# Kernel optimization log

Hardware: AMD Instinct MI355X
Metric: run time of the kernel (lower is better)

## Reference

```python
import jax, jax.numpy as jnp
import numpy as np
from jax import lax

EPS = 1e-5
DN = ('NCHW', 'OIHW', 'NCHW')

def _sign(v):
    # (v >= 0) * 2 - 1
    return jnp.where(v >= 0, 1.0, -1.0).astype(v.dtype)

def _conv(x, w, b):
    y = lax.conv_general_dilated(x, w, (1, 1), 'VALID', dimension_numbers=DN)
    return y + b[None, :, None, None]

def _bn(x):
    # BatchNorm2d(affine=False), training mode: biased batch stats over (N,H,W)
    m = jnp.mean(x, axis=(0, 2, 3), keepdims=True)
    v = jnp.var(x, axis=(0, 2, 3), keepdims=True)
    return (x - m) * lax.rsqrt(v + EPS)

def setup_inputs() -> dict:
    key = jax.random.key(0)
    ks = jax.random.split(key, 9)
    f = jnp.float32
    B = 8192
    x = jax.random.normal(ks[0], (B, 1, 28, 28), dtype=f)
    # conv params, clipped to [-1, 1] as in clip_weights()
    w1 = jnp.clip(jax.random.normal(ks[1], (32, 1, 9, 9), dtype=f) * 0.1, -1, 1)
    b1 = jnp.clip(jax.random.normal(ks[2], (32,), dtype=f) * 0.1, -1, 1)
    w2 = jnp.clip(jax.random.normal(ks[3], (16, 32, 9, 9), dtype=f) * 0.1, -1, 1)
    b2 = jnp.clip(jax.random.normal(ks[4], (16,), dtype=f) * 0.1, -1, 1)
    w3 = jnp.clip(jax.random.normal(ks[5], (8, 16, 9, 9), dtype=f) * 0.1, -1, 1)
    b3 = jnp.clip(jax.random.normal(ks[6], (8,), dtype=f) * 0.1, -1, 1)
    wl = jnp.clip(jax.random.normal(ks[7], (10, 8, 4, 4), dtype=f) * 0.1, -1, 1)
    bl = jnp.clip(jax.random.normal(ks[8], (10,), dtype=f) * 0.1, -1, 1)
    return {"x": x, "w1": w1, "b1": b1, "w2": w2, "b2": b2,
            "w3": w3, "b3": b3, "wl": wl, "bl": bl}

def _block(x, w, b, act=True, norm=True, binarized=True):
    if binarized:
        w, b = _sign(w), _sign(b)
    x = _conv(x, w, b)
    if norm:
        x = _bn(x)
    if act:
        x = _sign(x) if binarized else jax.nn.relu(x)
    return x

def reference(x, w1, b1, w2, b2, w3, b3, wl, bl):
    x = _sign(x)                        # binarize input activations
    x = _block(x, w1, b1)               # (B, 32, 20, 20)
    x = _block(x, w2, b2)               # (B, 16, 12, 12)
    x = _block(x, w3, b3)               # (B,  8,  4,  4)
    x = _block(x, wl, bl, act=False, norm=False)  # (B, 10, 1, 1), binarized weights
    return x.reshape(-1, 10)
```

## Files before the change

### kernel.cpp

```cpp
#include <hip/hip_runtime.h>
#include <stdint.h>

#define BATCH 8192

#define OFF_W1R3   0
#define OFF_W2P    384
#define OFF_W3P    6144
#define OFF_WLB    9600
#define OFF_SBL    9760
#define OFF_TTOT   9856
#define OFF_S3     10184
#define OFF_S2PART 10496
#define OFF_Z2     76800
#define OFF_Z3     37825792

__global__ __launch_bounds__(256) void k1_pack_tsum(const float* __restrict__ x,
                                                    const float* __restrict__ w1,
                                                    const float* __restrict__ w2,
                                                    const float* __restrict__ w3,
                                                    const float* __restrict__ wl,
                                                    const float* __restrict__ bl,
                                                    uint8_t* __restrict__ ws) {
  int* Ttot = (int*)(ws + OFF_TTOT);
  const int tid = threadIdx.x;

  if (blockIdx.x == 0) {
    uint32_t* W1R3 = (uint32_t*)(ws + OFF_W1R3);
    uint32_t* W2P  = (uint32_t*)(ws + OFF_W2P);
    uint32_t* W3P  = (uint32_t*)(ws + OFF_W3P);
    uint64_t* WLB  = (uint64_t*)(ws + OFF_WLB);
    float*    SBL  = (float*)(ws + OFF_SBL);
    for (int e = tid; e < 96; e += 256) {
      int oc = e / 3, i = e % 3;
      uint32_t m = 0;
      for (int rr = 0; rr < 3; ++rr)
        for (int kw = 0; kw < 9; ++kw)
          if (w1[oc*81 + (3*i+rr)*9 + kw] < 0.f) m |= 1u << (rr*9 + kw);
      W1R3[e] = m;
    }
    for (int e = tid; e < 648; e += 256) {
      int och = e / 81, k = e % 81;
      int kh = k / 9, kw = k % 9;
      uint32_t m0 = 0, m1 = 0;
      int oc0 = och*2;
      for (int ic = 0; ic < 32; ++ic) {
        if (w2[(oc0*32 + ic)*81 + k] < 0.f)     m0 |= 1u << ic;
        if (w2[((oc0+1)*32 + ic)*81 + k] < 0.f) m1 |= 1u << ic;
      }
      int idx = ((och*9 + kh)*10 + kw)*2;
      W2P[idx] = m0; W2P[idx+1] = m1;
    }
    for (int e = tid; e < 72; e += 256) {
      int idx = (e*10 + 9)*2;
      W2P[idx] = 0; W2P[idx+1] = 0;
    }
    for (int e = tid; e < 648; e += 256) {
      int oc = e / 81, k = e % 81;
      int kh = k / 9, kw = k % 9;
      uint32_t m = 0;
      for (int ic = 0; ic < 16; ++ic)
        if (w3[(oc*16 + ic)*81 + k] < 0.f) m |= 1u << ic;
      W3P[(oc*9 + kh)*12 + kw] = m;
    }
    for (int e = tid; e < 216; e += 256) {
      int row = e / 3, p = e % 3;
      W3P[row*12 + 9 + p] = 0;
    }
    for (int e = tid; e < 20; e += 256) {
      int oc = e >> 1, word = e & 1;
      uint64_t m = 0;
      for (int b = 0; b < 64; ++b)
        if (wl[oc*128 + word*64 + b] < 0.f) m |= 1ull << b;
      WLB[e] = m;
    }
    if (tid < 10) SBL[tid] = (bl[tid] >= 0.f) ? 1.f : -1.f;
  }

  __shared__ uint32_t rowm[224];
  __shared__ int Tacc[81];
  if (tid < 81) Tacc[tid] = 0;
  __syncthreads();

  const int img0 = blockIdx.x * 8;
  if (tid < 224) {
    int il = tid / 28, r = tid % 28;
    const float4* xr = (const float4*)(x + (size_t)(img0 + il) * 784 + r * 28);
    uint32_t m = 0;
    #pragma unroll
    for (int j = 0; j < 7; ++j) {
      float4 v = xr[j];
      if (v.x < 0.f) m |= 1u << (j*4+0);
      if (v.y < 0.f) m |= 1u << (j*4+1);
      if (v.z < 0.f) m |= 1u << (j*4+2);
      if (v.w < 0.f) m |= 1u << (j*4+3);
    }
    rowm[tid] = m;
  }
  __syncthreads();

  if (tid < 72) {
    int il = tid / 9, kw = tid % 9;
    int base = il * 28;
    int n9[9];
    int sum20 = 0;
    #pragma unroll
    for (int r = 0; r < 20; ++r) {
      int n = __popc((rowm[base + r] >> kw) & 0xFFFFFu);
      if (r < 9) n9[r] = n;
      sum20 += n;
    }
    atomicAdd(&Tacc[kw], 400 - 2*sum20);
    #pragma unroll
    for (int kh = 1; kh <= 8; ++kh) {
      int nadd = __popc((rowm[base + kh + 19] >> kw) & 0xFFFFFu);
      sum20 += nadd - n9[kh-1];
      atomicAdd(&Tacc[kh*9 + kw], 400 - 2*sum20);
    }
  }
  __syncthreads();
  if (tid < 81) atomicAdd(&Ttot[tid], Tacc[tid]);
}

#define K2_IMGS 8
__global__ __launch_bounds__(256) void k2_conv12(const float* __restrict__ x,
                                                 uint8_t* __restrict__ ws) {
  const uint32_t* W1R3g = (const uint32_t*)(ws + OFF_W1R3);
  const uint32_t* W2Pg  = (const uint32_t*)(ws + OFF_W2P);
  const int* Ttot = (const int*)(ws + OFF_TTOT);
  int* S2P = (int*)(ws + OFF_S2PART);

  __shared__ uint32_t __attribute__((aligned(16))) rowm[K2_IMGS*28];
  __shared__ uint32_t __attribute__((aligned(16))) w1r3[96];
  __shared__ uint32_t __attribute__((aligned(16))) w2p[1440];
  __shared__ int tlds[81];
  __shared__ int t1s[32];
  __shared__ uint32_t __attribute__((aligned(16))) A1s[K2_IMGS*400];
  __shared__ int s2acc[16];

  const int tid = threadIdx.x;
  const int img0 = blockIdx.x * K2_IMGS;

  for (int e = tid; e < 96; e += 256)   w1r3[e] = W1R3g[e];
  for (int e = tid; e < 1440; e += 256) w2p[e]  = W2Pg[e];
  if (tid < 81) tlds[tid] = Ttot[tid];
  if (tid < 16) s2acc[tid] = 0;
  if (tid < K2_IMGS*28) {
    int il = tid / 28, rr = tid % 28;
    const float4* xr = (const float4*)(x + (size_t)(img0 + il) * 784 + rr * 28);
    uint32_t m = 0;
    #pragma unroll
    for (int j = 0; j < 7; ++j) {
      float4 v = xr[j];
      if (v.x < 0.f) m |= 1u << (j*4+0);
      if (v.y < 0.f) m |= 1u << (j*4+1);
      if (v.z < 0.f) m |= 1u << (j*4+2);
      if (v.w < 0.f) m |= 1u << (j*4+3);
    }
    rowm[tid] = m;
  }
  __syncthreads();

  if (tid < 32) {
    long long S = 0;
    for (int kh = 0; kh < 9; ++kh)
      for (int kw = 0; kw < 9; ++kw) {
        int bit = (w1r3[tid*3 + kh/3] >> ((kh%3)*9 + kw)) & 1;
        S += (long long)(1 - 2*bit) * tlds[kh*9 + kw];
      }
    const long long N1 = (long long)BATCH * 400;
    long long q = S / N1, rr = S % N1;
    long long t = q + (rr > 0 ? 1 : 0);
    if ((t & 1) == 0) t += 1;
    t1s[tid] = (int)t;
  }
  __syncthreads();

  for (int G = tid; G < K2_IMGS*80; G += 256) {
    int il = G / 80, rem = G - il*80;
    int oh = rem >> 2, ow0 = (rem & 3) * 5;
    uint32_t R[9];
    #pragma unroll
    for (int i = 0; i < 9; ++i) R[i] = rowm[il*28 + oh + i];
    uint32_t win[5][3];
    #pragma unroll
    for (int j = 0; j < 5; ++j) {
      int ow = ow0 + j;
      #pragma unroll
      for (int i = 0; i < 3; ++i) {
        uint32_t b0 = (R[3*i]   >> ow) & 0x1FFu;
        uint32_t b1 = (R[3*i+1] >> ow) & 0x1FFu;
        uint32_t b2 = (R[3*i+2] >> ow) & 0x1FFu;
        win[j][i] = b0 | (b1 << 9) | (b2 << 18);
      }
    }
    uint32_t mask[5] = {0,0,0,0,0};
    #pragma unroll
    for (int ocg = 0; ocg < 4; ++ocg) {
      const uint4* wp = (const uint4*)&w1r3[ocg*24];
      uint32_t wr[24];
      #pragma unroll
      for (int q = 0; q < 6; ++q) {
        uint4 v = wp[q];
        wr[q*4+0]=v.x; wr[q*4+1]=v.y; wr[q*4+2]=v.z; wr[q*4+3]=v.w;
      }
      #pragma unroll
      for (int o8 = 0; o8 < 8; ++o8) {
        int oc = ocg*8 + o8;
        int t = t1s[oc];
        #pragma unroll
        for (int j = 0; j < 5; ++j) {
          int mm = __popc(win[j][0] ^ wr[o8*3])
                 + __popc(win[j][1] ^ wr[o8*3+1])
                 + __popc(win[j][2] ^ wr[o8*3+2]);
          mask[j] |= (uint32_t)((81 - 2*mm) < t) << oc;
        }
      }
    }
    #pragma unroll
    for (int j = 0; j < 5; ++j) A1s[il*400 + oh*20 + ow0 + j] = mask[j];
  }
  __syncthreads();

  uint32_t* Z2w = (uint32_t*)(ws + OFF_Z2);
  const int och = tid & 7, oc0 = och << 1;
  int sl0 = 0, sl1 = 0;
  for (int r = 0; r < 3; ++r) {
    int G = tid + r*256;
    int il = G / 96, rem = G - il*96;
    int oy = rem >> 3;
    const uint32_t* A = &A1s[il*400 + oy*20];
    int acc0[12], acc1[12];
    #pragma unroll
    for (int p = 0; p < 12; ++p) { acc0[p] = 0; acc1[p] = 0; }
    for (int kh = 0; kh < 9; ++kh) {
      const uint4* ar = (const uint4*)(A + kh*20);
      uint32_t a[20];
      #pragma unroll
      for (int q = 0; q < 5; ++q) {
        uint4 v = ar[q];
        a[q*4+0]=v.x; a[q*4+1]=v.y; a[q*4+2]=v.z; a[q*4+3]=v.w;
      }
      const uint4* wp4 = (const uint4*)&w2p[(och*9 + kh)*20];
      uint32_t wbuf[20];
      #pragma unroll
      for (int q = 0; q < 5; ++q) {
        uint4 v = wp4[q];
        wbuf[q*4+0]=v.x; wbuf[q*4+1]=v.y; wbuf[q*4+2]=v.z; wbuf[q*4+3]=v.w;
      }
      #pragma unroll
      for (int kw = 0; kw < 9; ++kw) {
        uint32_t w0 = wbuf[2*kw], w1v = wbuf[2*kw+1];
        #pragma unroll
        for (int px = 0; px < 12; ++px) {
          acc0[px] += __popc(a[kw+px] ^ w0);
          acc1[px] += __popc(a[kw+px] ^ w1v);
        }
      }
    }
    size_t wbase = (size_t)(img0+il)*1152 + (size_t)oy*96 + och;
    #pragma unroll
    for (int px = 0; px < 12; ++px) {
      int z0 = 2592 - 2*acc0[px], z1v = 2592 - 2*acc1[px];
      sl0 += z0; sl1 += z1v;
      Z2w[wbase + px*8] = (uint32_t)(uint16_t)(int16_t)z0
                        | ((uint32_t)(uint16_t)(int16_t)z1v << 16);
    }
  }
  atomicAdd(&s2acc[oc0],   sl0);
  atomicAdd(&s2acc[oc0+1], sl1);
  __syncthreads();
  if (tid < 16) S2P[blockIdx.x*16 + tid] = s2acc[tid];
}

#define K3_IMGS 8
__global__ __launch_bounds__(256) void k3_conv3(uint8_t* __restrict__ ws) {
  const int* S2P = (const int*)(ws + OFF_S2PART);
  const uint32_t* W3Pg = (const uint32_t*)(ws + OFF_W3P);
  const uint32_t* Z2w = (const uint32_t*)(ws + OFF_Z2);
  uint32_t* Z3w = (uint32_t*)(ws + OFF_Z3);
  unsigned long long* S3 = (unsigned long long*)(ws + OFF_S3);

  __shared__ uint32_t __attribute__((aligned(16))) w3p[864];
  __shared__ int part[256];
  __shared__ int t2s[16];
  __shared__ uint32_t __attribute__((aligned(16))) A2[K3_IMGS*144];
  __shared__ int s3acc[8];

  const int tid = threadIdx.x;
  const int img0 = blockIdx.x * K3_IMGS;

  {
    int c = tid & 15, g = tid >> 4;
    int s = 0;
    for (int j = 0; j < 64; ++j) s += S2P[(g + 16*j)*16 + c];
    part[tid] = s;
  }
  for (int e = tid; e < 864; e += 256) w3p[e] = W3Pg[e];
  if (tid < 8) s3acc[tid] = 0;
  __syncthreads();
  if (tid < 16) {
    long long S = 0;
    #pragma unroll
    for (int g = 0; g < 16; ++g) S += (long long)part[g*16 + tid];
    const long long N2 = (long long)BATCH * 144;
    long long q = S / N2, r = S % N2;
    long long t = q + (r > 0 ? 1 : 0);
    if (t & 1) t += 1;
    t2s[tid] = (int)t;
  }
  __syncthreads();

  for (int idx = tid; idx < K3_IMGS*144; idx += 256) {
    const uint4* zp = (const uint4*)&Z2w[(size_t)(img0 + idx/144)*1152 + (size_t)(idx%144)*8];
    uint4 v0 = zp[0], v1 = zp[1];
    uint32_t zz[8] = {v0.x,v0.y,v0.z,v0.w, v1.x,v1.y,v1.z,v1.w};
    uint32_t m = 0;
    #pragma unroll
    for (int i = 0; i < 8; ++i) {
      int zlo = (int)(short)(zz[i] & 0xFFFFu);
      int zhi = (int)zz[i] >> 16;
      m |= (uint32_t)(zlo < t2s[2*i])   << (2*i);
      m |= (uint32_t)(zhi < t2s[2*i+1]) << (2*i+1);
    }
    A2[idx] = m;
  }
  __syncthreads();

  const int il = tid >> 5, oc = (tid >> 2) & 7, oy = tid & 3;
  int acc[4] = {0, 0, 0, 0};
  #pragma unroll
  for (int kh = 0; kh < 9; ++kh) {
    const uint4* ar = (const uint4*)&A2[il*144 + (oy + kh)*12];
    uint4 v0 = ar[0], v1 = ar[1], v2 = ar[2];
    uint32_t a[12] = {v0.x,v0.y,v0.z,v0.w, v1.x,v1.y,v1.z,v1.w, v2.x,v2.y,v2.z,v2.w};
    const uint4* wr = (const uint4*)&w3p[(oc*9 + kh)*12];
    uint4 w0 = wr[0], w1v = wr[1], w2v = wr[2];
    uint32_t w[9] = {w0.x,w0.y,w0.z,w0.w, w1v.x,w1v.y,w1v.z,w1v.w, w2v.x};
    #pragma unroll
    for (int ox = 0; ox < 4; ++ox) {
      #pragma unroll
      for (int kw = 0; kw < 9; ++kw) acc[ox] += __popc(a[ox+kw] ^ w[kw]);
    }
  }
  int ssum = 0;
  uint32_t packed[2];
  #pragma unroll
  for (int h = 0; h < 2; ++h) {
    int za = 1296 - 2*acc[2*h], zb = 1296 - 2*acc[2*h+1];
    ssum += za + zb;
    packed[h] = (uint32_t)(uint16_t)(int16_t)za | ((uint32_t)(uint16_t)(int16_t)zb << 16);
  }
  *(uint2*)&Z3w[(size_t)(img0 + il)*64 + oc*8 + oy*2] = make_uint2(packed[0], packed[1]);
  atomicAdd(&s3acc[oc], ssum);
  __syncthreads();
  if (tid < 8)
    atomicAdd(&S3[tid], (unsigned long long)(long long)s3acc[tid]);
}

__global__ __launch_bounds__(64) void k4_final(uint8_t* __restrict__ ws,
                                               float* __restrict__ out) {
  const uint32_t* Z3w = (const uint32_t*)(ws + OFF_Z3);
  const long long* S3 = (const long long*)(ws + OFF_S3);
  const uint64_t* WLBg = (const uint64_t*)(ws + OFF_WLB);
  const float* SBLg = (const float*)(ws + OFF_SBL);
  __shared__ int t3[8];
  __shared__ uint64_t wlb[20];
  __shared__ float sbl[10];
  const int tid = threadIdx.x;
  if (tid < 8) {
    long long S = S3[tid];
    const long long N3 = (long long)BATCH * 16;
    long long q = S / N3, r = S % N3;
    long long t = q + (r > 0 ? 1 : 0);
    if (t & 1) t += 1;
    t3[tid] = (int)t;
  }
  if (tid < 20) wlb[tid] = WLBg[tid];
  if (tid < 10) sbl[tid] = SBLg[tid];
  __syncthreads();
  int img = blockIdx.x * 64 + tid;
  const uint4* zp = (const uint4*)&Z3w[(size_t)img * 64];
  uint32_t zz[64];
  #pragma unroll
  for (int q = 0; q < 16; ++q) {
    uint4 v = zp[q];
    zz[q*4+0]=v.x; zz[q*4+1]=v.y; zz[q*4+2]=v.z; zz[q*4+3]=v.w;
  }
  uint64_t a0 = 0, a1 = 0;
  #pragma unroll
  for (int j = 0; j < 64; ++j) {
    int z = (j & 1) ? ((int)zz[j>>1] >> 16) : (int)(short)(zz[j>>1] & 0xFFFFu);
    a0 |= (uint64_t)(z < t3[j >> 4]) << j;
  }
  #pragma unroll
  for (int j = 0; j < 64; ++j) {
    int z = (j & 1) ? ((int)zz[32 + (j>>1)] >> 16) : (int)(short)(zz[32 + (j>>1)] & 0xFFFFu);
    a1 |= (uint64_t)(z < t3[(64 + j) >> 4]) << j;
  }
  #pragma unroll
  for (int oc = 0; oc < 10; ++oc) {
    int mism = __popcll(a0 ^ wlb[oc*2]) + __popcll(a1 ^ wlb[oc*2 + 1]);
    out[(size_t)img*10 + oc] = (float)(128 - 2*mism) + sbl[oc];
  }
}

extern "C" void kernel_launch(void* const* d_in, const int* in_sizes, int n_in,
                              void* d_out, int out_size, void* d_ws, size_t ws_size,
                              hipStream_t stream) {
  (void)in_sizes; (void)n_in; (void)out_size; (void)ws_size;
  const float* x  = (const float*)d_in[0];
  const float* w1 = (const float*)d_in[1];
  const float* w2 = (const float*)d_in[3];
  const float* w3 = (const float*)d_in[5];
  const float* wl = (const float*)d_in[7];
  const float* bl = (const float*)d_in[8];
  uint8_t* ws = (uint8_t*)d_ws;
  float* out = (float*)d_out;

  hipMemsetAsync(ws + OFF_TTOT, 0, 400, stream);
  k1_pack_tsum<<<1024, 256, 0, stream>>>(x, w1, w2, w3, wl, bl, ws);
  k2_conv12<<<1024, 256, 0, stream>>>(x, ws);
  k3_conv3<<<1024, 256, 0, stream>>>(ws);
  k4_final<<<128, 64, 0, stream>>>(ws, out);
}
```

Measured before the change: 272.4 us.

## Fuse four BNN kernels into one cooperative persistent kernel with grid syncs

Replaces the four separate kernel launches and the memset with a single cooperative kernel. Blocks loop over virtual blocks and use grid.sync between the phases that need global batch-norm statistics. Global atomics for the stats are replaced by per-block partial arrays that each block reduces after the sync, and weight packing is split across four blocks. This removes launch gaps and the memset, at the cost of grid-wide barriers, redundant partial reductions in every block, and a shared-memory union sized for the largest phase, which may lower occupancy.

```diff
diff --git a/kernel.cpp b/kernel.cpp
--- a/kernel.cpp
+++ b/kernel.cpp
@@ -1,35 +1,74 @@
 #include <hip/hip_runtime.h>
+#include <hip/hip_cooperative_groups.h>
 #include <stdint.h>
 
+namespace cg = cooperative_groups;
+
 #define BATCH 8192
-
-#define OFF_W1R3   0
-#define OFF_W2P    384
-#define OFF_W3P    6144
-#define OFF_WLB    9600
-#define OFF_SBL    9760
-#define OFF_TTOT   9856
-#define OFF_S3     10184
-#define OFF_S2PART 10496
-#define OFF_Z2     76800
-#define OFF_Z3     37825792
-
-__global__ __launch_bounds__(256) void k1_pack_tsum(const float* __restrict__ x,
-                                                    const float* __restrict__ w1,
-                                                    const float* __restrict__ w2,
-                                                    const float* __restrict__ w3,
-                                                    const float* __restrict__ wl,
-                                                    const float* __restrict__ bl,
-                                                    uint8_t* __restrict__ ws) {
-  int* Ttot = (int*)(ws + OFF_TTOT);
+#define NVB   1024
+
+#define OFF_W1R3  0
+#define OFF_W2P   384
+#define OFF_W3P   6144
+#define OFF_WLB   9600
+#define OFF_SBL   9760
+#define OFF_TPART 9856
+#define OFF_S2P   341632
+#define OFF_S3P   407168
+#define OFF_Z2    440320
+#define OFF_Z3    38189056
+
+struct PhaseA { uint32_t rowm[224]; int Tacc[81]; };
+struct PhaseB { uint32_t rowm[224]; uint32_t w1r3[96]; uint32_t w2p[1440];
+                int red[256]; int tlds[81]; int t1s[32];
+                uint32_t A1s[3200]; int s2acc[16]; };
+struct PhaseC { uint32_t w3p[864]; int part[256]; int t2s[16]; int s3acc[8];
+                uint32_t A2[1152]; };
+struct PhaseD { int red[128]; int t3[8]; uint64_t wlb[20]; float sbl[10]; };
+union SMemU { PhaseA a; PhaseB b; PhaseC c; PhaseD d; };
+
+__global__ __launch_bounds__(256)
+void fused_bnn(const float* __restrict__ x,  const float* __restrict__ w1,
+               const float* __restrict__ w2, const float* __restrict__ w3,
+               const float* __restrict__ wl, const float* __restrict__ bl,
+               uint8_t* __restrict__ ws, float* __restrict__ out) {
+  cg::grid_group grid = cg::this_grid();
+  __shared__ __align__(16) SMemU sm;
   const int tid = threadIdx.x;
+  const int G = gridDim.x;
+
+  int* TPART = (int*)(ws + OFF_TPART);
+  int* S2P   = (int*)(ws + OFF_S2P);
+  int* S3P   = (int*)(ws + OFF_S3P);
+  uint32_t* Z2w = (uint32_t*)(ws + OFF_Z2);
+  uint32_t* Z3w = (uint32_t*)(ws + OFF_Z3);
 
   if (blockIdx.x == 0) {
+    uint32_t* W2P = (uint32_t*)(ws + OFF_W2P);
+    for (int e = tid; e < 648; e += 256) {
+      int och = e / 81, k = e % 81, kh = k / 9, kw = k % 9;
+      uint32_t m0 = 0, m1 = 0;
+      int oc0 = och * 2;
+      for (int ic = 0; ic < 32; ++ic) {
+        if (w2[(oc0*32 + ic)*81 + k] < 0.f)     m0 |= 1u << ic;
+        if (w2[((oc0+1)*32 + ic)*81 + k] < 0.f) m1 |= 1u << ic;
+      }
+      int idx = ((och*9 + kh)*10 + kw)*2;
+      W2P[idx] = m0; W2P[idx+1] = m1;
+    }
+    for (int e = tid; e < 72; e += 256) { int idx = (e*10 + 9)*2; W2P[idx] = 0; W2P[idx+1] = 0; }
+  } else if (blockIdx.x == 1) {
+    uint32_t* W3P = (uint32_t*)(ws + OFF_W3P);
+    for (int e = tid; e < 648; e += 256) {
+      int oc = e / 81, k = e % 81, kh = k / 9, kw = k % 9;
+      uint32_t m = 0;
+      for (int ic = 0; ic < 16; ++ic)
+        if (w3[(oc*16 + ic)*81 + k] < 0.f) m |= 1u << ic;
+      W3P[(oc*9 + kh)*12 + kw] = m;
+    }
+    for (int e = tid; e < 216; e += 256) { int row = e / 3, p = e % 3; W3P[row*12 + 9 + p] = 0; }
+  } else if (blockIdx.x == 2) {
     uint32_t* W1R3 = (uint32_t*)(ws + OFF_W1R3);
-    uint32_t* W2P  = (uint32_t*)(ws + OFF_W2P);
-    uint32_t* W3P  = (uint32_t*)(ws + OFF_W3P);
-    uint64_t* WLB  = (uint64_t*)(ws + OFF_WLB);
-    float*    SBL  = (float*)(ws + OFF_SBL);
     for (int e = tid; e < 96; e += 256) {
       int oc = e / 3, i = e % 3;
       uint32_t m = 0;
@@ -38,34 +77,9 @@
           if (w1[oc*81 + (3*i+rr)*9 + kw] < 0.f) m |= 1u << (rr*9 + kw);
       W1R3[e] = m;
     }
-    for (int e = tid; e < 648; e += 256) {
-      int och = e / 81, k = e % 81;
-      int kh = k / 9, kw = k % 9;
-      uint32_t m0 = 0, m1 = 0;
-      int oc0 = och*2;
-      for (int ic = 0; ic < 32; ++ic) {
-        if (w2[(oc0*32 + ic)*81 + k] < 0.f)     m0 |= 1u << ic;
-        if (w2[((oc0+1)*32 + ic)*81 + k] < 0.f) m1 |= 1u << ic;
-      }
-      int idx = ((och*9 + kh)*10 + kw)*2;
-      W2P[idx] = m0; W2P[idx+1] = m1;
-    }
-    for (int e = tid; e < 72; e += 256) {
-      int idx = (e*10 + 9)*2;
-      W2P[idx] = 0; W2P[idx+1] = 0;
-    }
-    for (int e = tid; e < 648; e += 256) {
-      int oc = e / 81, k = e % 81;
-      int kh = k / 9, kw = k % 9;
-      uint32_t m = 0;
-      for (int ic = 0; ic < 16; ++ic)
-        if (w3[(oc*16 + ic)*81 + k] < 0.f) m |= 1u << ic;
-      W3P[(oc*9 + kh)*12 + kw] = m;
-    }
-    for (int e = tid; e < 216; e += 256) {
-      int row = e / 3, p = e % 3;
-      W3P[row*12 + 9 + p] = 0;
-    }
+  } else if (blockIdx.x == 3) {
+    uint64_t* WLB = (uint64_t*)(ws + OFF_WLB);
+    float* SBL = (float*)(ws + OFF_SBL);
     for (int e = tid; e < 20; e += 256) {
       int oc = e >> 1, word = e & 1;
       uint64_t m = 0;
@@ -76,331 +90,328 @@
     if (tid < 10) SBL[tid] = (bl[tid] >= 0.f) ? 1.f : -1.f;
   }
 
-  __shared__ uint32_t rowm[224];
-  __shared__ int Tacc[81];
-  if (tid < 81) Tacc[tid] = 0;
-  __syncthreads();
-
-  const int img0 = blockIdx.x * 8;
-  if (tid < 224) {
-    int il = tid / 28, r = tid % 28;
-    const float4* xr = (const float4*)(x + (size_t)(img0 + il) * 784 + r * 28);
-    uint32_t m = 0;
-    #pragma unroll
-    for (int j = 0; j < 7; ++j) {
-      float4 v = xr[j];
-      if (v.x < 0.f) m |= 1u << (j*4+0);
-      if (v.y < 0.f) m |= 1u << (j*4+1);
-      if (v.z < 0.f) m |= 1u << (j*4+2);
-      if (v.w < 0.f) m |= 1u << (j*4+3);
-    }
-    rowm[tid] = m;
+  for (int vb = blockIdx.x; vb < NVB; vb += G) {
+    if (tid < 81) sm.a.Tacc[tid] = 0;
+    __syncthreads();
+    const int img0 = vb * 8;
+    if (tid < 224) {
+      int il = tid / 28, r = tid % 28;
+      const float4* xr = (const float4*)(x + (size_t)(img0 + il) * 784 + r * 28);
+      uint32_t m = 0;
+      #pragma unroll
+      for (int j = 0; j < 7; ++j) {
+        float4 v = xr[j];
+        if (v.x < 0.f) m |= 1u << (j*4+0);
+        if (v.y < 0.f) m |= 1u << (j*4+1);
+        if (v.z < 0.f) m |= 1u << (j*4+2);
+        if (v.w < 0.f) m |= 1u << (j*4+3);
+      }
+      sm.a.rowm[tid] = m;
+    }
+    __syncthreads();
+    if (tid < 72) {
+      int il = tid / 9, kw = tid % 9;
+      int base = il * 28;
+      int n9[9];
+      int sum20 = 0;
+      #pragma unroll
+      for (int r = 0; r < 20; ++r) {
+        int n = __popc((sm.a.rowm[base + r] >> kw) & 0xFFFFFu);
+        if (r < 9) n9[r] = n;
+        sum20 += n;
+      }
+      atomicAdd(&sm.a.Tacc[kw], 400 - 2*sum20);
+      #pragma unroll
+      for (int kh = 1; kh <= 8; ++kh) {
+        int nadd = __popc((sm.a.rowm[base + kh + 19] >> kw) & 0xFFFFFu);
+        sum20 += nadd - n9[kh-1];
+        atomicAdd(&sm.a.Tacc[kh*9 + kw], 400 - 2*sum20);
+      }
+    }
+    __syncthreads();
+    if (tid < 81) TPART[vb*81 + tid] = sm.a.Tacc[tid];
+    __syncthreads();
   }
-  __syncthreads();
-
-  if (tid < 72) {
-    int il = tid / 9, kw = tid % 9;
-    int base = il * 28;
-    int n9[9];
-    int sum20 = 0;
-    #pragma unroll
-    for (int r = 0; r < 20; ++r) {
-      int n = __popc((rowm[base + r] >> kw) & 0xFFFFFu);
-      if (r < 9) n9[r] = n;
-      sum20 += n;
-    }
-    atomicAdd(&Tacc[kw], 400 - 2*sum20);
-    #pragma unroll
-    for (int kh = 1; kh <= 8; ++kh) {
-      int nadd = __popc((rowm[base + kh + 19] >> kw) & 0xFFFFFu);
-      sum20 += nadd - n9[kh-1];
-      atomicAdd(&Tacc[kh*9 + kw], 400 - 2*sum20);
-    }
+  __threadfence();
+  grid.sync();
+
+  {
+    const uint32_t* W1R3g = (const uint32_t*)(ws + OFF_W1R3);
+    const uint32_t* W2Pg  = (const uint32_t*)(ws + OFF_W2P);
+    for (int e = tid; e < 96; e += 256)   sm.b.w1r3[e] = W1R3g[e];
+    for (int e = tid; e < 1440; e += 256) sm.b.w2p[e]  = W2Pg[e];
+    {
+      int s = 0;
+      if (tid < 243) {
+        int k = tid % 81, sub = tid / 81;
+        for (int r = sub; r < NVB; r += 3) s += TPART[r*81 + k];
+      }
+      sm.b.red[tid] = s;
+    }
+    __syncthreads();
+    if (tid < 81) sm.b.tlds[tid] = sm.b.red[tid] + sm.b.red[tid+81] + sm.b.red[tid+162];
+    __syncthreads();
+    if (tid < 32) {
+      long long S = 0;
+      for (int kh = 0; kh < 9; ++kh)
+        for (int kw = 0; kw < 9; ++kw) {
+          int bit = (sm.b.w1r3[tid*3 + kh/3] >> ((kh%3)*9 + kw)) & 1;
+          S += (long long)(1 - 2*bit) * sm.b.tlds[kh*9 + kw];
+        }
+      const long long N1 = (long long)BATCH * 400;
+      long long q = S / N1, rr = S % N1;
+      long long t = q + (rr > 0 ? 1 : 0);
+      if ((t & 1) == 0) t += 1;
+      sm.b.t1s[tid] = (int)t;
+    }
+    if (tid < 16) sm.b.s2acc[tid] = 0;
+    __syncthreads();
+
+    const int och = tid & 7, oc0 = och << 1;
+    for (int vb = blockIdx.x; vb < NVB; vb += G) {
+      const int img0 = vb * 8;
+      if (tid < 224) {
+        int il = tid / 28, rr = tid % 28;
+        const float4* xr = (const float4*)(x + (size_t)(img0 + il) * 784 + rr * 28);
+        uint32_t m = 0;
+        #pragma unroll
+        for (int j = 0; j < 7; ++j) {
+          float4 v = xr[j];
+          if (v.x < 0.f) m |= 1u << (j*4+0);
+          if (v.y < 0.f) m |= 1u << (j*4+1);
+          if (v.z < 0.f) m |= 1u << (j*4+2);
+          if (v.w < 0.f) m |= 1u << (j*4+3);
+        }
+        sm.b.rowm[tid] = m;
+      }
+      __syncthreads();
+
+      for (int Gt = tid; Gt < 640; Gt += 256) {
+        int il = Gt / 80, rem = Gt - il*80;
+        int oh = rem >> 2, ow0 = (rem & 3) * 5;
+        uint32_t R[9];
+        #pragma unroll
+        for (int i = 0; i < 9; ++i) R[i] = sm.b.rowm[il*28 + oh + i];
+        uint32_t win[5][3];
+        #pragma unroll
+        for (int j = 0; j < 5; ++j) {
+          int ow = ow0 + j;
+          #pragma unroll
+          for (int i = 0; i < 3; ++i) {
+            uint32_t b0 = (R[3*i]   >> ow) & 0x1FFu;
+            uint32_t b1 = (R[3*i+1] >> ow) & 0x1FFu;
+            uint32_t b2 = (R[3*i+2] >> ow) & 0x1FFu;
+            win[j][i] = b0 | (b1 << 9) | (b2 << 18);
+          }
+        }
+        uint32_t mask[5] = {0,0,0,0,0};
+        #pragma unroll
+        for (int ocg = 0; ocg < 4; ++ocg) {
+          const uint4* wp = (const uint4*)&sm.b.w1r3[ocg*24];
+          uint32_t wr[24];
+          #pragma unroll
+          for (int q = 0; q < 6; ++q) {
+            uint4 v = wp[q];
+            wr[q*4+0]=v.x; wr[q*4+1]=v.y; wr[q*4+2]=v.z; wr[q*4+3]=v.w;
+          }
+          #pragma unroll
+          for (int o8 = 0; o8 < 8; ++o8) {
+            int oc = ocg*8 + o8;
+            int t = sm.b.t1s[oc];
+            #pragma unroll
+            for (int j = 0; j < 5; ++j) {
+              int mm = __popc(win[j][0] ^ wr[o8*3])
+                     + __popc(win[j][1] ^ wr[o8*3+1])
+                     + __popc(win[j][2] ^ wr[o8*3+2]);
+              mask[j] |= (uint32_t)((81 - 2*mm) < t) << oc;
+            }
+          }
+        }
+        #pragma unroll
+        for (int j = 0; j < 5; ++j) sm.b.A1s[il*400 + oh*20 + ow0 + j] = mask[j];
+      }
+      __syncthreads();
+
+      int sl0 = 0, sl1 = 0;
+      for (int r = 0; r < 3; ++r) {
+        int Gt = tid + r*256;
+        int il = Gt / 96, rem = Gt - il*96;
+        int oy = rem >> 3;
+        const uint32_t* A = &sm.b.A1s[il*400 + oy*20];
+        int acc0[12], acc1[12];
+        #pragma unroll
+        for (int p = 0; p < 12; ++p) { acc0[p] = 0; acc1[p] = 0; }
+        for (int kh = 0; kh < 9; ++kh) {
+          const uint4* ar = (const uint4*)(A + kh*20);
+          uint32_t a[20];
+          #pragma unroll
+          for (int q = 0; q < 5; ++q) {
+            uint4 v = ar[q];
+            a[q*4+0]=v.x; a[q*4+1]=v.y; a[q*4+2]=v.z; a[q*4+3]=v.w;
+          }
+          const uint4* wp4 = (const uint4*)&sm.b.w2p[(och*9 + kh)*20];
+          uint32_t wbuf[20];
+          #pragma unroll
+          for (int q = 0; q < 5; ++q) {
+            uint4 v = wp4[q];
+            wbuf[q*4+0]=v.x; wbuf[q*4+1]=v.y; wbuf[q*4+2]=v.z; wbuf[q*4+3]=v.w;
+          }
+          #pragma unroll
+          for (int kw = 0; kw < 9; ++kw) {
+            uint32_t w0 = wbuf[2*kw], w1v = wbuf[2*kw+1];
+            #pragma unroll
+            for (int px = 0; px < 12; ++px) {
+              acc0[px] += __popc(a[kw+px] ^ w0);
+              acc1[px] += __popc(a[kw+px] ^ w1v);
+            }
+          }
+        }
+        size_t wbase = (size_t)(img0+il)*1152 + (size_t)oy*96 + och;
+        #pragma unroll
+        for (int px = 0; px < 12; ++px) {
+          int z0 = 2592 - 2*acc0[px], z1v = 2592 - 2*acc1[px];
+          sl0 += z0; sl1 += z1v;
+          Z2w[wbase + px*8] = (uint32_t)(uint16_t)(int16_t)z0
+                            | ((uint32_t)(uint16_t)(int16_t)z1v << 16);
+        }
+      }
+      atomicAdd(&sm.b.s2acc[oc0],   sl0);
+      atomicAdd(&sm.b.s2acc[oc0+1], sl1);
+      __syncthreads();
+    }
+    if (tid < 16) S2P[blockIdx.x*16 + tid] = sm.b.s2acc[tid];
   }
-  __syncthreads();
-  if (tid < 81) atomicAdd(&Ttot[tid], Tacc[tid]);
-}
-
-#define K2_IMGS 8
-__global__ __launch_bounds__(256) void k2_conv12(const float* __restrict__ x,
-                                                 uint8_t* __restrict__ ws) {
-  const uint32_t* W1R3g = (const uint32_t*)(ws + OFF_W1R3);
-  const uint32_t* W2Pg  = (const uint32_t*)(ws + OFF_W2P);
-  const int* Ttot = (const int*)(ws + OFF_TTOT);
-  int* S2P = (int*)(ws + OFF_S2PART);
-
-  __shared__ uint32_t __attribute__((aligned(16))) rowm[K2_IMGS*28];
-  __shared__ uint32_t __attribute__((aligned(16))) w1r3[96];
-  __shared__ uint32_t __attribute__((aligned(16))) w2p[1440];
-  __shared__ int tlds[81];
-  __shared__ int t1s[32];
-  __shared__ uint32_t __attribute__((aligned(16))) A1s[K2_IMGS*400];
-  __shared__ int s2acc[16];
-
-  const int tid = threadIdx.x;
-  const int img0 = blockIdx.x * K2_IMGS;
-
-  for (int e = tid; e < 96; e += 256)   w1r3[e] = W1R3g[e];
-  for (int e = tid; e < 1440; e += 256) w2p[e]  = W2Pg[e];
-  if (tid < 81) tlds[tid] = Ttot[tid];
-  if (tid < 16) s2acc[tid] = 0;
-  if (tid < K2_IMGS*28) {
-    int il = tid / 28, rr = tid % 28;
-    const float4* xr = (const float4*)(x + (size_t)(img0 + il) * 784 + rr * 28);
-    uint32_t m = 0;
-    #pragma unroll
-    for (int j = 0; j < 7; ++j) {
-      float4 v = xr[j];
-      if (v.x < 0.f) m |= 1u << (j*4+0);
-      if (v.y < 0.f) m |= 1u << (j*4+1);
-      if (v.z < 0.f) m |= 1u << (j*4+2);
-      if (v.w < 0.f) m |= 1u << (j*4+3);
-    }
-    rowm[tid] = m;
+  __threadfence();
+  grid.sync();
+
+  {
+    const uint32_t* W3Pg = (const uint32_t*)(ws + OFF_W3P);
+    {
+      int c = tid & 15, g = tid >> 4;
+      int s = 0;
+      for (int b = g; b < G; b += 16) s += S2P[b*16 + c];
+      sm.c.part[tid] = s;
+    }
+    for (int e = tid; e < 864; e += 256) sm.c.w3p[e] = W3Pg[e];
+    if (tid < 8) sm.c.s3acc[tid] = 0;
+    __syncthreads();
+    if (tid < 16) {
+      long long S = 0;
+      #pragma unroll
+      for (int g = 0; g < 16; ++g) S += (long long)sm.c.part[g*16 + tid];
+      const long long N2 = (long long)BATCH * 144;
+      long long q = S / N2, r = S % N2;
+      long long t = q + (r > 0 ? 1 : 0);
+      if (t & 1) t += 1;
+      sm.c.t2s[tid] = (int)t;
+    }
+    __syncthreads();
+
+    for (int vb = blockIdx.x; vb < NVB; vb += G) {
+      const int img0 = vb * 8;
+      for (int idx = tid; idx < 1152; idx += 256) {
+        const uint4* zp = (const uint4*)&Z2w[(size_t)(img0 + idx/144)*1152 + (size_t)(idx%144)*8];
+        uint4 v0 = zp[0], v1 = zp[1];
+        uint32_t zz[8] = {v0.x,v0.y,v0.z,v0.w, v1.x,v1.y,v1.z,v1.w};
+        uint32_t m = 0;
+        #pragma unroll
+        for (int i = 0; i < 8; ++i) {
+          int zlo = (int)(short)(zz[i] & 0xFFFFu);
+          int zhi = (int)zz[i] >> 16;
+          m |= (uint32_t)(zlo < sm.c.t2s[2*i])   << (2*i);
+          m |= (uint32_t)(zhi < sm.c.t2s[2*i+1]) << (2*i+1);
+        }
+        sm.c.A2[idx] = m;
+      }
+      __syncthreads();
+      {
+        const int il = tid >> 5, oc = (tid >> 2) & 7, oy = tid & 3;
+        int acc[4] = {0, 0, 0, 0};
+        #pragma unroll
+        for (int kh = 0; kh < 9; ++kh) {
+          const uint4* ar = (const uint4*)&sm.c.A2[il*144 + (oy + kh)*12];
+          uint4 v0 = ar[0], v1 = ar[1], v2 = ar[2];
+          uint32_t a[12] = {v0.x,v0.y,v0.z,v0.w, v1.x,v1.y,v1.z,v1.w, v2.x,v2.y,v2.z,v2.w};
+          const uint4* wr = (const uint4*)&sm.c.w3p[(oc*9 + kh)*12];
+          uint4 w0 = wr[0], w1v = wr[1], w2v = wr[2];
+          uint32_t w[9] = {w0.x,w0.y,w0.z,w0.w, w1v.x,w1v.y,w1v.z,w1v.w, w2v.x};
+          #pragma unroll
+          for (int ox = 0; ox < 4; ++ox) {
+            #pragma unroll
+            for (int kw = 0; kw < 9; ++kw) acc[ox] += __popc(a[ox+kw] ^ w[kw]);
+          }
+        }
+        int ssum = 0;
+        uint32_t packed[2];
+        #pragma unroll
+        for (int h = 0; h < 2; ++h) {
+          int za = 1296 - 2*acc[2*h], zb = 1296 - 2*acc[2*h+1];
+          ssum += za + zb;
+          packed[h] = (uint32_t)(uint16_t)(int16_t)za | ((uint32_t)(uint16_t)(int16_t)zb << 16);
+        }
+        *(uint2*)&Z3w[(size_t)(img0 + il)*64 + oc*8 + oy*2] = make_uint2(packed[0], packed[1]);
+        atomicAdd(&sm.c.s3acc[oc], ssum);
+      }
+      __syncthreads();
+    }
+    if (tid < 8) S3P[blockIdx.x*8 + tid] = sm.c.s3acc[tid];
   }
-  __syncthreads();
-
-  if (tid < 32) {
-    long long S = 0;
-    for (int kh = 0; kh < 9; ++kh)
-      for (int kw = 0; kw < 9; ++kw) {
-        int bit = (w1r3[tid*3 + kh/3] >> ((kh%3)*9 + kw)) & 1;
-        S += (long long)(1 - 2*bit) * tlds[kh*9 + kw];
-      }
-    const long long N1 = (long long)BATCH * 400;
-    long long q = S / N1, rr = S % N1;
-    long long t = q + (rr > 0 ? 1 : 0);
-    if ((t & 1) == 0) t += 1;
-    t1s[tid] = (int)t;
-  }
-  __syncthreads();
-
-  for (int G = tid; G < K2_IMGS*80; G += 256) {
-    int il = G / 80, rem = G - il*80;
-    int oh = rem >> 2, ow0 = (rem & 3) * 5;
-    uint32_t R[9];
-    #pragma unroll
-    for (int i = 0; i < 9; ++i) R[i] = rowm[il*28 + oh + i];
-    uint32_t win[5][3];
-    #pragma unroll
-    for (int j = 0; j < 5; ++j) {
-      int ow = ow0 + j;
-      #pragma unroll
-      for (int i = 0; i < 3; ++i) {
-        uint32_t b0 = (R[3*i]   >> ow) & 0x1FFu;
-        uint32_t b1 = (R[3*i+1] >> ow) & 0x1FFu;
-        uint32_t b2 = (R[3*i+2] >> ow) & 0x1FFu;
-        win[j][i] = b0 | (b1 << 9) | (b2 << 18);
-      }
-    }
-    uint32_t mask[5] = {0,0,0,0,0};
-    #pragma unroll
-    for (int ocg = 0; ocg < 4; ++ocg) {
-      const uint4* wp = (const uint4*)&w1r3[ocg*24];
-      uint32_t wr[24];
-      #pragma unroll
-      for (int q = 0; q < 6; ++q) {
-        uint4 v = wp[q];
-        wr[q*4+0]=v.x; wr[q*4+1]=v.y; wr[q*4+2]=v.z; wr[q*4+3]=v.w;
-      }
-      #pragma unroll
-      for (int o8 = 0; o8 < 8; ++o8) {
-        int oc = ocg*8 + o8;
-        int t = t1s[oc];
-        #pragma unroll
-        for (int j = 0; j < 5; ++j) {
-          int mm = __popc(win[j][0] ^ wr[o8*3])
-                 + __popc(win[j][1] ^ wr[o8*3+1])
-                 + __popc(win[j][2] ^ wr[o8*3+2]);
-          mask[j] |= (uint32_t)((81 - 2*mm) < t) << oc;
-        }
-      }
-    }
-    #pragma unroll
-    for (int j = 0; j < 5; ++j) A1s[il*400 + oh*20 + ow0 + j] = mask[j];
-  }
-  __syncthreads();
-
-  uint32_t* Z2w = (uint32_t*)(ws + OFF_Z2);
-  const int och = tid & 7, oc0 = och << 1;
-  int sl0 = 0, sl1 = 0;
-  for (int r = 0; r < 3; ++r) {
-    int G = tid + r*256;
-    int il = G / 96, rem = G - il*96;
-    int oy = rem >> 3;
-    const uint32_t* A = &A1s[il*400 + oy*20];
-    int acc0[12], acc1[12];
-    #pragma unroll
-    for (int p = 0; p < 12; ++p) { acc0[p] = 0; acc1[p] = 0; }
-    for (int kh = 0; kh < 9; ++kh) {
-      const uint4* ar = (const uint4*)(A + kh*20);
-      uint32_t a[20];
-      #pragma unroll
-      for (int q = 0; q < 5; ++q) {
-        uint4 v = ar[q];
-        a[q*4+0]=v.x; a[q*4+1]=v.y; a[q*4+2]=v.z; a[q*4+3]=v.w;
-      }
-      const uint4* wp4 = (const uint4*)&w2p[(och*9 + kh)*20];
-      uint32_t wbuf[20];
-      #pragma unroll
-      for (int q = 0; q < 5; ++q) {
-        uint4 v = wp4[q];
-        wbuf[q*4+0]=v.x; wbuf[q*4+1]=v.y; wbuf[q*4+2]=v.z; wbuf[q*4+3]=v.w;
-      }
-      #pragma unroll
-      for (int kw = 0; kw < 9; ++kw) {
-        uint32_t w0 = wbuf[2*kw], w1v = wbuf[2*kw+1];
-        #pragma unroll
-        for (int px = 0; px < 12; ++px) {
-          acc0[px] += __popc(a[kw+px] ^ w0);
-          acc1[px] += __popc(a[kw+px] ^ w1v);
-        }
-      }
-    }
-    size_t wbase = (size_t)(img0+il)*1152 + (size_t)oy*96 + och;
-    #pragma unroll
-    for (int px = 0; px < 12; ++px) {
-      int z0 = 2592 - 2*acc0[px], z1v = 2592 - 2*acc1[px];
-      sl0 += z0; sl1 += z1v;
-      Z2w[wbase + px*8] = (uint32_t)(uint16_t)(int16_t)z0
-                        | ((uint32_t)(uint16_t)(int16_t)z1v << 16);
-    }
-  }
-  atomicAdd(&s2acc[oc0],   sl0);
-  atomicAdd(&s2acc[oc0+1], sl1);
-  __syncthreads();
-  if (tid < 16) S2P[blockIdx.x*16 + tid] = s2acc[tid];
-}
-
-#define K3_IMGS 8
-__global__ __launch_bounds__(256) void k3_conv3(uint8_t* __restrict__ ws) {
-  const int* S2P = (const int*)(ws + OFF_S2PART);
-  const uint32_t* W3Pg = (const uint32_t*)(ws + OFF_W3P);
-  const uint32_t* Z2w = (const uint32_t*)(ws + OFF_Z2);
-  uint32_t* Z3w = (uint32_t*)(ws + OFF_Z3);
-  unsigned long long* S3 = (unsigned long long*)(ws + OFF_S3);
-
-  __shared__ uint32_t __attribute__((aligned(16))) w3p[864];
-  __shared__ int part[256];
-  __shared__ int t2s[16];
-  __shared__ uint32_t __attribute__((aligned(16))) A2[K3_IMGS*144];
-  __shared__ int s3acc[8];
-
-  const int tid = threadIdx.x;
-  const int img0 = blockIdx.x * K3_IMGS;
+  __threadfence();
+  grid.sync();
 
   {
-    int c = tid & 15, g = tid >> 4;
-    int s = 0;
-    for (int j = 0; j < 64; ++j) s += S2P[(g + 16*j)*16 + c];
-    part[tid] = s;
-  }
-  for (int e = tid; e < 864; e += 256) w3p[e] = W3Pg[e];
-  if (tid < 8) s3acc[tid] = 0;
-  __syncthreads();
-  if (tid < 16) {
-    long long S = 0;
-    #pragma unroll
-    for (int g = 0; g < 16; ++g) S += (long long)part[g*16 + tid];
-    const long long N2 = (long long)BATCH * 144;
-    long long q = S / N2, r = S % N2;
-    long long t = q + (r > 0 ? 1 : 0);
-    if (t & 1) t += 1;
-    t2s[tid] = (int)t;
-  }
-  __syncthreads();
-
-  for (int idx = tid; idx < K3_IMGS*144; idx += 256) {
-    const uint4* zp = (const uint4*)&Z2w[(size_t)(img0 + idx/144)*1152 + (size_t)(idx%144)*8];
-    uint4 v0 = zp[0], v1 = zp[1];
-    uint32_t zz[8] = {v0.x,v0.y,v0.z,v0.w, v1.x,v1.y,v1.z,v1.w};
-    uint32_t m = 0;
-    #pragma unroll
-    for (int i = 0; i < 8; ++i) {
-      int zlo = (int)(short)(zz[i] & 0xFFFFu);
-      int zhi = (int)zz[i] >> 16;
-      m |= (uint32_t)(zlo < t2s[2*i])   << (2*i);
-      m |= (uint32_t)(zhi < t2s[2*i+1]) << (2*i+1);
-    }
-    A2[idx] = m;
-  }
-  __syncthreads();
-
-  const int il = tid >> 5, oc = (tid >> 2) & 7, oy = tid & 3;
-  int acc[4] = {0, 0, 0, 0};
-  #pragma unroll
-  for (int kh = 0; kh < 9; ++kh) {
-    const uint4* ar = (const uint4*)&A2[il*144 + (oy + kh)*12];
-    uint4 v0 = ar[0], v1 = ar[1], v2 = ar[2];
-    uint32_t a[12] = {v0.x,v0.y,v0.z,v0.w, v1.x,v1.y,v1.z,v1.w, v2.x,v2.y,v2.z,v2.w};
-    const uint4* wr = (const uint4*)&w3p[(oc*9 + kh)*12];
-    uint4 w0 = wr[0], w1v = wr[1], w2v = wr[2];
-    uint32_t w[9] = {w0.x,w0.y,w0.z,w0.w, w1v.x,w1v.y,w1v.z,w1v.w, w2v.x};
-    #pragma unroll
-    for (int ox = 0; ox < 4; ++ox) {
-      #pragma unroll
-      for (int kw = 0; kw < 9; ++kw) acc[ox] += __popc(a[ox+kw] ^ w[kw]);
-    }
-  }
-  int ssum = 0;
-  uint32_t packed[2];
-  #pragma unroll
-  for (int h = 0; h < 2; ++h) {
-    int za = 1296 - 2*acc[2*h], zb = 1296 - 2*acc[2*h+1];
-    ssum += za + zb;
-    packed[h] = (uint32_t)(uint16_t)(int16_t)za | ((uint32_t)(uint16_t)(int16_t)zb << 16);
-  }
-  *(uint2*)&Z3w[(size_t)(img0 + il)*64 + oc*8 + oy*2] = make_uint2(packed[0], packed[1]);
-  atomicAdd(&s3acc[oc], ssum);
-  __syncthreads();
-  if (tid < 8)
-    atomicAdd(&S3[tid], (unsigned long long)(long long)s3acc[tid]);
-}
-
-__global__ __launch_bounds__(64) void k4_final(uint8_t* __restrict__ ws,
-                                               float* __restrict__ out) {
-  const uint32_t* Z3w = (const uint32_t*)(ws + OFF_Z3);
-  const long long* S3 = (const long long*)(ws + OFF_S3);
-  const uint64_t* WLBg = (const uint64_t*)(ws + OFF_WLB);
-  const float* SBLg = (const float*)(ws + OFF_SBL);
-  __shared__ int t3[8];
-  __shared__ uint64_t wlb[20];
-  __shared__ float sbl[10];
-  const int tid = threadIdx.x;
-  if (tid < 8) {
-    long long S = S3[tid];
-    const long long N3 = (long long)BATCH * 16;
-    long long q = S / N3, r = S % N3;
-    long long t = q + (r > 0 ? 1 : 0);
-    if (t & 1) t += 1;
-    t3[tid] = (int)t;
-  }
-  if (tid < 20) wlb[tid] = WLBg[tid];
-  if (tid < 10) sbl[tid] = SBLg[tid];
-  __syncthreads();
-  int img = blockIdx.x * 64 + tid;
-  const uint4* zp = (const uint4*)&Z3w[(size_t)img * 64];
-  uint32_t zz[64];
-  #pragma unroll
-  for (int q = 0; q < 16; ++q) {
-    uint4 v = zp[q];
-    zz[q*4+0]=v.x; zz[q*4+1]=v.y; zz[q*4+2]=v.z; zz[q*4+3]=v.w;
-  }
-  uint64_t a0 = 0, a1 = 0;
-  #pragma unroll
-  for (int j = 0; j < 64; ++j) {
-    int z = (j & 1) ? ((int)zz[j>>1] >> 16) : (int)(short)(zz[j>>1] & 0xFFFFu);
-    a0 |= (uint64_t)(z < t3[j >> 4]) << j;
-  }
-  #pragma unroll
-  for (int j = 0; j < 64; ++j) {
-    int z = (j & 1) ? ((int)zz[32 + (j>>1)] >> 16) : (int)(short)(zz[32 + (j>>1)] & 0xFFFFu);
-    a1 |= (uint64_t)(z < t3[(64 + j) >> 4]) << j;
-  }
-  #pragma unroll
-  for (int oc = 0; oc < 10; ++oc) {
-    int mism = __popcll(a0 ^ wlb[oc*2]) + __popcll(a1 ^ wlb[oc*2 + 1]);
-    out[(size_t)img*10 + oc] = (float)(128 - 2*mism) + sbl[oc];
+    {
+      int s = 0;
+      if (tid < 128) {
+        int oc = tid & 7, g = tid >> 3;
+        for (int b = g; b < G; b += 16) s += S3P[b*8 + oc];
+        sm.d.red[tid] = s;
+      }
+    }
+    if (tid >= 128 && tid < 148) sm.d.wlb[tid - 128] = ((const uint64_t*)(ws + OFF_WLB))[tid - 128];
+    if (tid >= 160 && tid < 170) sm.d.sbl[tid - 160] = ((const float*)(ws + OFF_SBL))[tid - 160];
+    __syncthreads();
+    if (tid < 8) {
+      long long S = 0;
+      #pragma unroll
+      for (int g = 0; g < 16; ++g) S += (long long)sm.d.red[g*8 + tid];
+      const long long N3 = (long long)BATCH * 16;
+      long long q = S / N3, r = S % N3;
+      long long t = q + (r > 0 ? 1 : 0);
+      if (t & 1) t += 1;
+      sm.d.t3[tid] = (int)t;
+    }
+    __syncthreads();
+
+    for (int img = blockIdx.x*256 + tid; img < BATCH; img += G*256) {
+      const uint4* zp = (const uint4*)&Z3w[(size_t)img * 64];
+      uint64_t a0 = 0, a1 = 0;
+      #pragma unroll
+      for (int q = 0; q < 4; ++q) {
+        uint32_t mm = 0;
+        #pragma unroll
+        for (int i = 0; i < 4; ++i) {
+          uint4 v = zp[q*4 + i];
+          uint32_t w4[4] = {v.x, v.y, v.z, v.w};
+          #pragma unroll
+          for (int j = 0; j < 4; ++j) {
+            int word = q*16 + i*4 + j;
+            int th = sm.d.t3[word >> 3];
+            int zlo = (int)(short)(w4[j] & 0xFFFFu);
+            int zhi = (int)w4[j] >> 16;
+            mm |= (uint32_t)(zlo < th) << (2*(i*4+j));
+            mm |= (uint32_t)(zhi < th) << (2*(i*4+j)+1);
+          }
+        }
+        if (q < 2) a0 |= (uint64_t)mm << (32*q);
+        else       a1 |= (uint64_t)mm << (32*(q-2));
+      }
+      #pragma unroll
+      for (int oc = 0; oc < 10; ++oc) {
+        int mism = __popcll(a0 ^ sm.d.wlb[oc*2]) + __popcll(a1 ^ sm.d.wlb[oc*2 + 1]);
+        out[(size_t)img*10 + oc] = (float)(128 - 2*mism) + sm.d.sbl[oc];
+      }
+    }
   }
 }
 
@@ -417,9 +428,13 @@
   uint8_t* ws = (uint8_t*)d_ws;
   float* out = (float*)d_out;
 
-  hipMemsetAsync(ws + OFF_TTOT, 0, 400, stream);
-  k1_pack_tsum<<<1024, 256, 0, stream>>>(x, w1, w2, w3, wl, bl, ws);
-  k2_conv12<<<1024, 256, 0, stream>>>(x, ws);
-  k3_conv3<<<1024, 256, 0, stream>>>(ws);
-  k4_final<<<128, 64, 0, stream>>>(ws, out);
+  int nb = 0;
+  if (hipOccupancyMaxActiveBlocksPerMultiprocessor(&nb, fused_bnn, 256, 0) != hipSuccess || nb < 1)
+    nb = 2;
+  long long Gl = (long long)nb * 256;
+  int G = (int)(Gl > NVB ? NVB : Gl);
+
+  void* args[8] = {(void*)&x, (void*)&w1, (void*)&w2, (void*)&w3,
+                   (void*)&wl, (void*)&bl, (void*)&ws, (void*)&out};
+  hipLaunchCooperativeKernel((const void*)fused_bnn, dim3(G), dim3(256), args, 0, stream);
 }
```

Result: slower. 502.7 us (+84.6%).

## Replace global atomics with per-block partials and spread weight packing across blocks

Applied to the files above, without the earlier changes.

Weight packing, previously done serially by block 0 of k1, is split across blocks 0-8, and the final-layer weights are packed with wavefront ballots. The global atomic reductions for the first-layer tap sums and the layer-3 channel sums become per-block partial arrays, which the next kernel reduces redundantly in each block. This removes the memset launch and contention on a few global atomic addresses, and stops block 0 from being a straggler. In exchange, every k2 block now reads about 330KB of partials and every k4 block reads 32KB, which adds redundant global traffic.

```diff
diff --git a/kernel.cpp b/kernel.cpp
--- a/kernel.cpp
+++ b/kernel.cpp
@@ -2,17 +2,18 @@
 #include <stdint.h>
 
 #define BATCH 8192
-
-#define OFF_W1R3   0
-#define OFF_W2P    384
-#define OFF_W3P    6144
-#define OFF_WLB    9600
-#define OFF_SBL    9760
-#define OFF_TTOT   9856
-#define OFF_S3     10184
-#define OFF_S2PART 10496
-#define OFF_Z2     76800
-#define OFF_Z3     37825792
+#define NVB   1024
+
+#define OFF_W1R3  0
+#define OFF_W2P   384
+#define OFF_W3P   6144
+#define OFF_WLB   9600
+#define OFF_SBL   9760
+#define OFF_TPART 9856
+#define OFF_S2P   341632
+#define OFF_S3P   407168
+#define OFF_Z2    440320
+#define OFF_Z3    38189056
 
 __global__ __launch_bounds__(256) void k1_pack_tsum(const float* __restrict__ x,
                                                     const float* __restrict__ w1,
@@ -21,28 +22,18 @@
                                                     const float* __restrict__ wl,
                                                     const float* __restrict__ bl,
                                                     uint8_t* __restrict__ ws) {
-  int* Ttot = (int*)(ws + OFF_TTOT);
   const int tid = threadIdx.x;
-
-  if (blockIdx.x == 0) {
-    uint32_t* W1R3 = (uint32_t*)(ws + OFF_W1R3);
-    uint32_t* W2P  = (uint32_t*)(ws + OFF_W2P);
-    uint32_t* W3P  = (uint32_t*)(ws + OFF_W3P);
-    uint64_t* WLB  = (uint64_t*)(ws + OFF_WLB);
-    float*    SBL  = (float*)(ws + OFF_SBL);
-    for (int e = tid; e < 96; e += 256) {
-      int oc = e / 3, i = e % 3;
-      uint32_t m = 0;
-      for (int rr = 0; rr < 3; ++rr)
-        for (int kw = 0; kw < 9; ++kw)
-          if (w1[oc*81 + (3*i+rr)*9 + kw] < 0.f) m |= 1u << (rr*9 + kw);
-      W1R3[e] = m;
-    }
-    for (int e = tid; e < 648; e += 256) {
-      int och = e / 81, k = e % 81;
-      int kh = k / 9, kw = k % 9;
+  const int bid = blockIdx.x;
+  int* TPART = (int*)(ws + OFF_TPART);
+
+  if (bid < 4) {
+    uint32_t* W2P = (uint32_t*)(ws + OFF_W2P);
+    int e = bid * 162 + tid;
+    if (tid < 162) {
+      int och = e / 81, k = e % 81, kh = k / 9, kw = k % 9;
       uint32_t m0 = 0, m1 = 0;
-      int oc0 = och*2;
+      int oc0 = och * 2;
+      #pragma unroll
       for (int ic = 0; ic < 32; ++ic) {
         if (w2[(oc0*32 + ic)*81 + k] < 0.f)     m0 |= 1u << ic;
         if (w2[((oc0+1)*32 + ic)*81 + k] < 0.f) m1 |= 1u << ic;
@@ -50,28 +41,43 @@
       int idx = ((och*9 + kh)*10 + kw)*2;
       W2P[idx] = m0; W2P[idx+1] = m1;
     }
-    for (int e = tid; e < 72; e += 256) {
-      int idx = (e*10 + 9)*2;
+    if (bid == 0 && tid < 72) {
+      int idx = (tid*10 + 9)*2;
       W2P[idx] = 0; W2P[idx+1] = 0;
     }
-    for (int e = tid; e < 648; e += 256) {
-      int oc = e / 81, k = e % 81;
-      int kh = k / 9, kw = k % 9;
+  } else if (bid < 7) {
+    uint32_t* W3P = (uint32_t*)(ws + OFF_W3P);
+    int e = (bid - 4) * 216 + tid;
+    if (tid < 216) {
+      int oc = e / 81, k = e % 81, kh = k / 9, kw = k % 9;
       uint32_t m = 0;
+      #pragma unroll
       for (int ic = 0; ic < 16; ++ic)
         if (w3[(oc*16 + ic)*81 + k] < 0.f) m |= 1u << ic;
       W3P[(oc*9 + kh)*12 + kw] = m;
     }
-    for (int e = tid; e < 216; e += 256) {
-      int row = e / 3, p = e % 3;
-      W3P[row*12 + 9 + p] = 0;
-    }
-    for (int e = tid; e < 20; e += 256) {
-      int oc = e >> 1, word = e & 1;
-      uint64_t m = 0;
-      for (int b = 0; b < 64; ++b)
-        if (wl[oc*128 + word*64 + b] < 0.f) m |= 1ull << b;
-      WLB[e] = m;
+    if (bid == 4 && tid < 216) { int row = tid / 3, p = tid % 3; W3P[row*12 + 9 + p] = 0; }
+  } else if (bid == 7) {
+    uint32_t* W1R3 = (uint32_t*)(ws + OFF_W1R3);
+    if (tid < 96) {
+      int oc = tid / 3, i = tid % 3;
+      uint32_t m = 0;
+      #pragma unroll
+      for (int rr = 0; rr < 3; ++rr)
+        #pragma unroll
+        for (int kw = 0; kw < 9; ++kw)
+          if (w1[oc*81 + (3*i+rr)*9 + kw] < 0.f) m |= 1u << (rr*9 + kw);
+      W1R3[tid] = m;
+    }
+  } else if (bid == 8) {
+    uint64_t* WLB = (uint64_t*)(ws + OFF_WLB);
+    float* SBL = (float*)(ws + OFF_SBL);
+    #pragma unroll
+    for (int i = 0; i < 5; ++i) {
+      int idx = i*256 + tid;
+      float v = wl[idx];
+      unsigned long long m = __ballot(v < 0.f);
+      if ((tid & 63) == 0) WLB[idx >> 6] = m;
     }
     if (tid < 10) SBL[tid] = (bl[tid] >= 0.f) ? 1.f : -1.f;
   }
@@ -80,8 +86,7 @@
   __shared__ int Tacc[81];
   if (tid < 81) Tacc[tid] = 0;
   __syncthreads();
-
-  const int img0 = blockIdx.x * 8;
+  const int img0 = bid * 8;
   if (tid < 224) {
     int il = tid / 28, r = tid % 28;
     const float4* xr = (const float4*)(x + (size_t)(img0 + il) * 784 + r * 28);
@@ -97,7 +102,6 @@
     rowm[tid] = m;
   }
   __syncthreads();
-
   if (tid < 72) {
     int il = tid / 9, kw = tid % 9;
     int base = il * 28;
@@ -118,7 +122,7 @@
     }
   }
   __syncthreads();
-  if (tid < 81) atomicAdd(&Ttot[tid], Tacc[tid]);
+  if (tid < 81) TPART[bid*81 + tid] = Tacc[tid];
 }
 
 #define K2_IMGS 8
@@ -126,12 +130,13 @@
                                                  uint8_t* __restrict__ ws) {
   const uint32_t* W1R3g = (const uint32_t*)(ws + OFF_W1R3);
   const uint32_t* W2Pg  = (const uint32_t*)(ws + OFF_W2P);
-  const int* Ttot = (const int*)(ws + OFF_TTOT);
-  int* S2P = (int*)(ws + OFF_S2PART);
+  const int* TPART = (const int*)(ws + OFF_TPART);
+  int* S2P = (int*)(ws + OFF_S2P);
 
   __shared__ uint32_t __attribute__((aligned(16))) rowm[K2_IMGS*28];
   __shared__ uint32_t __attribute__((aligned(16))) w1r3[96];
   __shared__ uint32_t __attribute__((aligned(16))) w2p[1440];
+  __shared__ int red[243];
   __shared__ int tlds[81];
   __shared__ int t1s[32];
   __shared__ uint32_t __attribute__((aligned(16))) A1s[K2_IMGS*400];
@@ -142,7 +147,12 @@
 
   for (int e = tid; e < 96; e += 256)   w1r3[e] = W1R3g[e];
   for (int e = tid; e < 1440; e += 256) w2p[e]  = W2Pg[e];
-  if (tid < 81) tlds[tid] = Ttot[tid];
+  if (tid < 243) {
+    int k = tid % 81, sub = tid / 81;
+    int s = 0;
+    for (int r = sub; r < NVB; r += 3) s += TPART[r*81 + k];
+    red[tid] = s;
+  }
   if (tid < 16) s2acc[tid] = 0;
   if (tid < K2_IMGS*28) {
     int il = tid / 28, rr = tid % 28;
@@ -158,6 +168,8 @@
     }
     rowm[tid] = m;
   }
+  __syncthreads();
+  if (tid < 81) tlds[tid] = red[tid] + red[tid+81] + red[tid+162];
   __syncthreads();
 
   if (tid < 32) {
@@ -274,11 +286,11 @@
 
 #define K3_IMGS 8
 __global__ __launch_bounds__(256) void k3_conv3(uint8_t* __restrict__ ws) {
-  const int* S2P = (const int*)(ws + OFF_S2PART);
+  const int* S2P = (const int*)(ws + OFF_S2P);
   const uint32_t* W3Pg = (const uint32_t*)(ws + OFF_W3P);
   const uint32_t* Z2w = (const uint32_t*)(ws + OFF_Z2);
   uint32_t* Z3w = (uint32_t*)(ws + OFF_Z3);
-  unsigned long long* S3 = (unsigned long long*)(ws + OFF_S3);
+  int* S3P = (int*)(ws + OFF_S3P);
 
   __shared__ uint32_t __attribute__((aligned(16))) w3p[864];
   __shared__ int part[256];
@@ -353,30 +365,39 @@
   *(uint2*)&Z3w[(size_t)(img0 + il)*64 + oc*8 + oy*2] = make_uint2(packed[0], packed[1]);
   atomicAdd(&s3acc[oc], ssum);
   __syncthreads();
-  if (tid < 8)
-    atomicAdd(&S3[tid], (unsigned long long)(long long)s3acc[tid]);
+  if (tid < 8) S3P[blockIdx.x*8 + tid] = s3acc[tid];
 }
 
 __global__ __launch_bounds__(64) void k4_final(uint8_t* __restrict__ ws,
                                                float* __restrict__ out) {
   const uint32_t* Z3w = (const uint32_t*)(ws + OFF_Z3);
-  const long long* S3 = (const long long*)(ws + OFF_S3);
+  const int* S3P = (const int*)(ws + OFF_S3P);
   const uint64_t* WLBg = (const uint64_t*)(ws + OFF_WLB);
   const float* SBLg = (const float*)(ws + OFF_SBL);
+  __shared__ int red[64];
   __shared__ int t3[8];
   __shared__ uint64_t wlb[20];
   __shared__ float sbl[10];
   const int tid = threadIdx.x;
+  {
+    int oc = tid & 7, g = tid >> 3;
+    int s = 0;
+    for (int b = g; b < NVB; b += 8) s += S3P[b*8 + oc];
+    red[tid] = s;
+  }
+  if (tid < 20) wlb[tid] = WLBg[tid];
+  if (tid >= 32 && tid < 42) sbl[tid - 32] = SBLg[tid - 32];
+  __syncthreads();
   if (tid < 8) {
-    long long S = S3[tid];
+    long long S = 0;
+    #pragma unroll
+    for (int g = 0; g < 8; ++g) S += (long long)red[g*8 + tid];
     const long long N3 = (long long)BATCH * 16;
     long long q = S / N3, r = S % N3;
     long long t = q + (r > 0 ? 1 : 0);
     if (t & 1) t += 1;
     t3[tid] = (int)t;
   }
-  if (tid < 20) wlb[tid] = WLBg[tid];
-  if (tid < 10) sbl[tid] = SBLg[tid];
   __syncthreads();
   int img = blockIdx.x * 64 + tid;
   const uint4* zp = (const uint4*)&Z3w[(size_t)img * 64];
@@ -417,7 +438,6 @@
   uint8_t* ws = (uint8_t*)d_ws;
   float* out = (float*)d_out;
 
-  hipMemsetAsync(ws + OFF_TTOT, 0, 400, stream);
   k1_pack_tsum<<<1024, 256, 0, stream>>>(x, w1, w2, w3, wl, bl, ws);
   k2_conv12<<<1024, 256, 0, stream>>>(x, ws);
   k3_conv3<<<1024, 256, 0, stream>>>(ws);
```

Measured after the change: 318.1 us. +16.8%, slower.
